# Optimization experiments

Measured on AMD Instinct MI355X. Metric: run time of the kernel, lower is better.

## Reference

```python
import jax, jax.numpy as jnp
import numpy as np
from jax import lax

KH, KW = 3, 3
STRIDE = 1
PAD = 1


def setup_inputs() -> dict:
    key = jax.random.key(0)
    k1, k2, k3 = jax.random.split(key, 3)
    x = jax.random.normal(k1, (16, 256, 56, 56), dtype=jnp.float32)
    # pruned weight after reinit_weight(): shape (n_kept, out_c)
    weight = jax.random.normal(k2, (1152, 256), dtype=jnp.float32) * 0.05
    # kept im2col row indices (sorted, in [0, C*kh*kw))
    idx = jnp.sort(jax.random.randint(k3, (1152,), 0, 256 * KH * KW)).astype(jnp.int32)
    return {"x": x, "weight": weight, "idx": idx}


def reference(x, weight, idx):
    N, C, H, W = x.shape
    out_h = (H + 2 * PAD - KH) // STRIDE + 1
    out_w = (W + 2 * PAD - KW) // STRIDE + 1
    out_c = weight.shape[1]
    # im2col: patches is [N, C*KH*KW, out_h, out_w]; channel flatten order is
    # (C, kh, kw), matching the original permute(1, 4, 5, 0, 2, 3).
    patches = lax.conv_general_dilated_patches(
        x, (KH, KW), (STRIDE, STRIDE), [(PAD, PAD), (PAD, PAD)]
    )
    col = patches.transpose(1, 0, 2, 3).reshape(C * KH * KW, N * out_h * out_w)
    # prune rows (irregular gather) then GEMM with pruned weight
    x_tile = col[idx, :].T                      # [N*out_h*out_w, n_kept]
    conv_out = x_tile @ weight                  # [N*out_h*out_w, out_c]
    # reshape to NCHW as in original
    out = conv_out.reshape(N, out_h * out_w, out_c).transpose(0, 2, 1)
    return out.reshape(N, out_c, out_h, out_w)
```

## Files before the change

kernel.cpp:

```cpp
#include <hip/hip_runtime.h>

typedef __attribute__((ext_vector_type(8))) short short8;
typedef __attribute__((ext_vector_type(4))) float f32x4;
typedef __attribute__((ext_vector_type(4))) int i32x4;

typedef __attribute__((address_space(1))) const unsigned int gas_u32;
typedef __attribute__((address_space(3))) unsigned int las_u32;

#define HW 56
#define P_IMG 3136
#define XSTRIDE 802816
#define OUT_C 256
#define K_TOT 1152
#define KT_N 18
#define BM 128
#define NBLK 392

__device__ __forceinline__ unsigned short f2bf_bits(float f) {
    unsigned u = __builtin_bit_cast(unsigned, f);
    return (unsigned short)((u + 0x7FFFu + ((u >> 16) & 1u)) >> 16);
}

__global__ __launch_bounds__(256) void prep_w_kernel(const float* __restrict__ w,
                                                     unsigned short* __restrict__ gw) {
    int i = blockIdx.x * 256 + threadIdx.x;
    int e = i & 63;
    int oc = (i >> 6) & 255;
    int t = i >> 14;
    int ksrc = t * 64 + (e ^ ((oc & 7) << 3));
    gw[i] = f2bf_bits(w[ksrc * 256 + oc]);
}

__global__ __launch_bounds__(256) void prep_idx_kernel(const int* __restrict__ idx,
                                                       int* __restrict__ didx) {
    int i = blockIdx.x * 256 + threadIdx.x;
    if (i < K_TOT) {
        int v = idx[i];
        int c = v / 9;
        int rr = v - c * 9;
        int dh = rr / 3;
        int dw = rr - dh * 3;
        int delta_b = c * P_IMG + (dh - 1) * HW + (dw - 1) + 57;
        didx[i] = delta_b | (rr << 20);
    }
}

__global__ __launch_bounds__(512, 2) void mconv_mfma(
        const float* __restrict__ x,
        const unsigned short* __restrict__ gw,
        const int* __restrict__ didx,
        float* __restrict__ out) {
    __shared__ __attribute__((aligned(16))) char smem[98304];
    char* const A0 = smem;
    char* const A1 = smem + 16384;
    char* const W0 = smem + 32768;
    char* const W1 = smem + 65536;

    const int tid = threadIdx.x;
    const int wv  = tid >> 6;
    const int ln  = tid & 63;
    const int lhi = ln >> 4;
    const int llo = ln & 15;
    const int oc0 = (wv >> 1) * 64;
    const int mw0 = (wv & 1) * 64;

    const int bid = blockIdx.x;
    const int m0 = ((bid & 7) * 49 + (bid >> 3)) * BM;

    const int sr = tid >> 2;
    const int sq = tid & 3;
    const int mrow = m0 + sr;
    const int nimg = mrow / P_IMG;
    const int p = mrow - nimg * P_IMG;
    const int oh = p / HW;
    const int ow = p - oh * HW;
    const int gbase = nimg * XSTRIDE + p - 57;
    const int ohm1 = oh - 1, owm1 = ow - 1;

    unsigned oklut = 0;
    #pragma unroll
    for (int dh = 0; dh < 3; ++dh)
        #pragma unroll
        for (int dw = 0; dw < 3; ++dw) {
            bool okh = (unsigned)(ohm1 + dh) < (unsigned)HW;
            bool okw = (unsigned)(owm1 + dw) < (unsigned)HW;
            if (okh && okw) oklut |= (1u << (dh * 3 + dw));
        }

    {
        float tv[16];
        unsigned okm = 0;
        const int kbase = sq * 16;
        #pragma unroll
        for (int q4 = 0; q4 < 4; ++q4) {
            i32x4 d = *(const i32x4*)(didx + kbase + q4 * 4);
            int vvv[4] = { d.x, d.y, d.z, d.w };
            #pragma unroll
            for (int jj = 0; jj < 4; ++jj) {
                int j = q4 * 4 + jj;
                int v = vvv[jj];
                int addr = gbase + (v & 0xFFFFF);
                unsigned ok = (oklut >> (v >> 20)) & 1u;
                tv[j] = x[ok ? addr : 0];
                okm |= ok << j;
            }
        }
        #pragma unroll
        for (int rd = 0; rd < 4; ++rd) {
            const char* g = (const char*)gw + rd * 8192 + tid * 16;
            __builtin_amdgcn_global_load_lds((gas_u32*)g, (las_u32*)(W0 + rd * 8192 + tid * 16), 16, 0, 0);
        }
        short8 pk0, pk1;
        #pragma unroll
        for (int j = 0; j < 8; ++j) {
            pk0[j] = (short)(((okm >> j) & 1u) ? f2bf_bits(tv[j]) : (unsigned short)0);
            pk1[j] = (short)(((okm >> (j + 8)) & 1u) ? f2bf_bits(tv[j + 8]) : (unsigned short)0);
        }
        const int swz = (sr & 7) << 4;
        char* rowp = A0 + sr * 128;
        *(short8*)(rowp + ((sq * 32) ^ swz)) = pk0;
        *(short8*)(rowp + ((sq * 32 + 16) ^ swz)) = pk1;
    }
    __syncthreads();

    f32x4 acc[4][4] = {};

    for (int kt = 0; kt < KT_N; ++kt) {
        char* const Ac = (kt & 1) ? A1 : A0;
        char* const An = (kt & 1) ? A0 : A1;
        char* const Wc = (kt & 1) ? W1 : W0;
        char* const Wn = (kt & 1) ? W0 : W1;

        float tv[16];
        unsigned okm = 0;
        const bool do_stage = (kt + 1 < KT_N);
        if (do_stage) {
            const int kbase = (kt + 1) * 64 + sq * 16;
            #pragma unroll
            for (int q4 = 0; q4 < 4; ++q4) {
                i32x4 d = *(const i32x4*)(didx + kbase + q4 * 4);
                int vvv[4] = { d.x, d.y, d.z, d.w };
                #pragma unroll
                for (int jj = 0; jj < 4; ++jj) {
                    int j = q4 * 4 + jj;
                    int v = vvv[jj];
                    int addr = gbase + (v & 0xFFFFF);
                    unsigned ok = (oklut >> (v >> 20)) & 1u;
                    tv[j] = x[ok ? addr : 0];
                    okm |= ok << j;
                }
            }
            #pragma unroll
            for (int rd = 0; rd < 4; ++rd) {
                const char* g = (const char*)gw + (kt + 1) * 32768 + rd * 8192 + tid * 16;
                __builtin_amdgcn_global_load_lds((gas_u32*)g, (las_u32*)(Wn + rd * 8192 + tid * 16), 16, 0, 0);
            }
        }
        __builtin_amdgcn_sched_barrier(0);

        #pragma unroll
        for (int ks = 0; ks < 2; ++ks) {
            short8 wf[4], af[4];
            #pragma unroll
            for (int i = 0; i < 4; ++i) {
                const int row = oc0 + i * 16 + llo;
                wf[i] = *(const short8*)(Wc + row * 128 + ((ks * 64 + lhi * 16) ^ ((row & 7) << 4)));
            }
            #pragma unroll
            for (int i = 0; i < 4; ++i) {
                const int row = mw0 + i * 16 + llo;
                af[i] = *(const short8*)(Ac + row * 128 + ((ks * 64 + lhi * 16) ^ ((row & 7) << 4)));
            }
            #pragma unroll
            for (int ni = 0; ni < 4; ++ni)
                #pragma unroll
                for (int mi = 0; mi < 4; ++mi)
                    acc[ni][mi] = __builtin_amdgcn_mfma_f32_16x16x32_bf16(wf[ni], af[mi], acc[ni][mi], 0, 0, 0);
        }

        if (do_stage) {
            short8 pk0, pk1;
            #pragma unroll
            for (int j = 0; j < 8; ++j) {
                pk0[j] = (short)(((okm >> j) & 1u) ? f2bf_bits(tv[j]) : (unsigned short)0);
                pk1[j] = (short)(((okm >> (j + 8)) & 1u) ? f2bf_bits(tv[j + 8]) : (unsigned short)0);
            }
            const int swz = (sr & 7) << 4;
            char* rowp = An + sr * 128;
            *(short8*)(rowp + ((sq * 32) ^ swz)) = pk0;
            *(short8*)(rowp + ((sq * 32 + 16) ^ swz)) = pk1;
        }
        __syncthreads();
    }

    #pragma unroll
    for (int mi = 0; mi < 4; ++mi) {
        const int mg = m0 + mw0 + mi * 16 + llo;
        const int n = mg / P_IMG;
        const int pp = mg - n * P_IMG;
        float* ob = out + n * XSTRIDE + pp;
        #pragma unroll
        for (int ni = 0; ni < 4; ++ni) {
            const int ocb = (oc0 + ni * 16 + lhi * 4) * P_IMG;
            #pragma unroll
            for (int j = 0; j < 4; ++j)
                ob[ocb + j * P_IMG] = acc[ni][mi][j];
        }
    }
}

extern "C" void kernel_launch(void* const* d_in, const int* in_sizes, int n_in,
                              void* d_out, int out_size, void* d_ws, size_t ws_size,
                              hipStream_t stream) {
    const float* x  = (const float*)d_in[0];
    const float* w  = (const float*)d_in[1];
    const int* idx  = (const int*)d_in[2];
    float* out = (float*)d_out;

    unsigned short* gw = (unsigned short*)d_ws;
    int* didx = (int*)((char*)d_ws + K_TOT * OUT_C * 2);

    prep_w_kernel<<<dim3(1152), dim3(256), 0, stream>>>(w, gw);
    prep_idx_kernel<<<dim3(5), dim3(256), 0, stream>>>(idx, didx);
    mconv_mfma<<<dim3(NBLK), dim3(512), 0, stream>>>(x, gw, didx, out);
}
```

Baseline: 189.5 us.

## Halve M tile, read weight fragments straight from global, drop weight LDS staging

The M tile per block shrinks from 128 to 64 rows and the grid doubles to 784 blocks. Shared memory drops from 96KB to 16KB and the launch bound now asks for 4 blocks per CU. Weight fragments are no longer staged into LDS with global_load_lds; the prep kernel writes them in an MFMA-fragment-friendly packed layout and each wave loads them directly from global/L2 every k-step. The aim is higher occupancy and less LDS traffic and footprint, at the cost of more repeated global weight reads and lower MFMA reuse per A-tile.

```diff
diff --git a/kernel.cpp b/kernel.cpp
--- a/kernel.cpp
+++ b/kernel.cpp
@@ -3,9 +3,6 @@
 typedef __attribute__((ext_vector_type(8))) short short8;
 typedef __attribute__((ext_vector_type(4))) float f32x4;
 typedef __attribute__((ext_vector_type(4))) int i32x4;
-
-typedef __attribute__((address_space(1))) const unsigned int gas_u32;
-typedef __attribute__((address_space(3))) unsigned int las_u32;
 
 #define HW 56
 #define P_IMG 3136
@@ -13,8 +10,8 @@
 #define OUT_C 256
 #define K_TOT 1152
 #define KT_N 18
-#define BM 128
-#define NBLK 392
+#define BM 64
+#define NBLK 784
 
 __device__ __forceinline__ unsigned short f2bf_bits(float f) {
     unsigned u = __builtin_bit_cast(unsigned, f);
@@ -24,11 +21,13 @@
 __global__ __launch_bounds__(256) void prep_w_kernel(const float* __restrict__ w,
                                                      unsigned short* __restrict__ gw) {
     int i = blockIdx.x * 256 + threadIdx.x;
-    int e = i & 63;
-    int oc = (i >> 6) & 255;
-    int t = i >> 14;
-    int ksrc = t * 64 + (e ^ ((oc & 7) << 3));
-    gw[i] = f2bf_bits(w[ksrc * 256 + oc]);
+    int oc = i & 255;
+    int s = i >> 8;
+    short8 pk;
+    #pragma unroll
+    for (int j = 0; j < 8; ++j)
+        pk[j] = (short)f2bf_bits(w[(s * 8 + j) * 256 + oc]);
+    *(short8*)(gw + s * 2048 + oc * 8) = pk;
 }
 
 __global__ __launch_bounds__(256) void prep_idx_kernel(const int* __restrict__ idx,
@@ -45,16 +44,14 @@
     }
 }
 
-__global__ __launch_bounds__(512, 2) void mconv_mfma(
+__global__ __launch_bounds__(512, 4) void mconv_mfma(
         const float* __restrict__ x,
         const unsigned short* __restrict__ gw,
         const int* __restrict__ didx,
         float* __restrict__ out) {
-    __shared__ __attribute__((aligned(16))) char smem[98304];
+    __shared__ __attribute__((aligned(16))) char smem[16384];
     char* const A0 = smem;
-    char* const A1 = smem + 16384;
-    char* const W0 = smem + 32768;
-    char* const W1 = smem + 65536;
+    char* const A1 = smem + 8192;
 
     const int tid = threadIdx.x;
     const int wv  = tid >> 6;
@@ -62,13 +59,13 @@
     const int lhi = ln >> 4;
     const int llo = ln & 15;
     const int oc0 = (wv >> 1) * 64;
-    const int mw0 = (wv & 1) * 64;
+    const int mw0 = (wv & 1) * 32;
 
     const int bid = blockIdx.x;
-    const int m0 = ((bid & 7) * 49 + (bid >> 3)) * BM;
+    const int m0 = ((bid & 7) * 98 + (bid >> 3)) * BM;
 
-    const int sr = tid >> 2;
-    const int sq = tid & 3;
+    const int sr = tid >> 3;
+    const int sq = tid & 7;
     const int mrow = m0 + sr;
     const int nimg = mrow / P_IMG;
     const int p = mrow - nimg * P_IMG;
@@ -87,114 +84,90 @@
             if (okh && okw) oklut |= (1u << (dh * 3 + dw));
         }
 
+    const int swz = (sr & 7) << 4;
+    char* const rowp0 = A0 + sr * 128;
+    char* const rowp1 = A1 + sr * 128;
+
     {
-        float tv[16];
+        float tv[8];
         unsigned okm = 0;
-        const int kbase = sq * 16;
+        const int kbase = sq * 8;
+        i32x4 d0 = *(const i32x4*)(didx + kbase);
+        i32x4 d1 = *(const i32x4*)(didx + kbase + 4);
+        int vv[8] = { d0.x, d0.y, d0.z, d0.w, d1.x, d1.y, d1.z, d1.w };
         #pragma unroll
-        for (int q4 = 0; q4 < 4; ++q4) {
-            i32x4 d = *(const i32x4*)(didx + kbase + q4 * 4);
-            int vvv[4] = { d.x, d.y, d.z, d.w };
+        for (int j = 0; j < 8; ++j) {
+            int v = vv[j];
+            int addr = gbase + (v & 0xFFFFF);
+            unsigned ok = (oklut >> (v >> 20)) & 1u;
+            tv[j] = x[ok ? addr : 0];
+            okm |= ok << j;
+        }
+        short8 pk;
+        #pragma unroll
+        for (int j = 0; j < 8; ++j)
+            pk[j] = (short)(((okm >> j) & 1u) ? f2bf_bits(tv[j]) : (unsigned short)0);
+        *(short8*)(rowp0 + ((sq * 16) ^ swz)) = pk;
+    }
+    __syncthreads();
+
+    f32x4 acc[4][2] = {};
+
+    for (int kt = 0; kt < KT_N; ++kt) {
+        char* const Ac = (kt & 1) ? A1 : A0;
+        char* const rowpn = (kt & 1) ? rowp0 : rowp1;
+
+        float tv[8];
+        unsigned okm = 0;
+        const bool do_stage = (kt + 1 < KT_N);
+        if (do_stage) {
+            const int kbase = (kt + 1) * 64 + sq * 8;
+            i32x4 d0 = *(const i32x4*)(didx + kbase);
+            i32x4 d1 = *(const i32x4*)(didx + kbase + 4);
+            int vv[8] = { d0.x, d0.y, d0.z, d0.w, d1.x, d1.y, d1.z, d1.w };
             #pragma unroll
-            for (int jj = 0; jj < 4; ++jj) {
-                int j = q4 * 4 + jj;
-                int v = vvv[jj];
+            for (int j = 0; j < 8; ++j) {
+                int v = vv[j];
                 int addr = gbase + (v & 0xFFFFF);
                 unsigned ok = (oklut >> (v >> 20)) & 1u;
                 tv[j] = x[ok ? addr : 0];
                 okm |= ok << j;
             }
         }
-        #pragma unroll
-        for (int rd = 0; rd < 4; ++rd) {
-            const char* g = (const char*)gw + rd * 8192 + tid * 16;
-            __builtin_amdgcn_global_load_lds((gas_u32*)g, (las_u32*)(W0 + rd * 8192 + tid * 16), 16, 0, 0);
-        }
-        short8 pk0, pk1;
-        #pragma unroll
-        for (int j = 0; j < 8; ++j) {
-            pk0[j] = (short)(((okm >> j) & 1u) ? f2bf_bits(tv[j]) : (unsigned short)0);
-            pk1[j] = (short)(((okm >> (j + 8)) & 1u) ? f2bf_bits(tv[j + 8]) : (unsigned short)0);
-        }
-        const int swz = (sr & 7) << 4;
-        char* rowp = A0 + sr * 128;
-        *(short8*)(rowp + ((sq * 32) ^ swz)) = pk0;
-        *(short8*)(rowp + ((sq * 32 + 16) ^ swz)) = pk1;
-    }
-    __syncthreads();
-
-    f32x4 acc[4][4] = {};
-
-    for (int kt = 0; kt < KT_N; ++kt) {
-        char* const Ac = (kt & 1) ? A1 : A0;
-        char* const An = (kt & 1) ? A0 : A1;
-        char* const Wc = (kt & 1) ? W1 : W0;
-        char* const Wn = (kt & 1) ? W0 : W1;
-
-        float tv[16];
-        unsigned okm = 0;
-        const bool do_stage = (kt + 1 < KT_N);
-        if (do_stage) {
-            const int kbase = (kt + 1) * 64 + sq * 16;
-            #pragma unroll
-            for (int q4 = 0; q4 < 4; ++q4) {
-                i32x4 d = *(const i32x4*)(didx + kbase + q4 * 4);
-                int vvv[4] = { d.x, d.y, d.z, d.w };
-                #pragma unroll
-                for (int jj = 0; jj < 4; ++jj) {
-                    int j = q4 * 4 + jj;
-                    int v = vvv[jj];
-                    int addr = gbase + (v & 0xFFFFF);
-                    unsigned ok = (oklut >> (v >> 20)) & 1u;
-                    tv[j] = x[ok ? addr : 0];
-                    okm |= ok << j;
-                }
-            }
-            #pragma unroll
-            for (int rd = 0; rd < 4; ++rd) {
-                const char* g = (const char*)gw + (kt + 1) * 32768 + rd * 8192 + tid * 16;
-                __builtin_amdgcn_global_load_lds((gas_u32*)g, (las_u32*)(Wn + rd * 8192 + tid * 16), 16, 0, 0);
-            }
-        }
         __builtin_amdgcn_sched_barrier(0);
 
         #pragma unroll
         for (int ks = 0; ks < 2; ++ks) {
-            short8 wf[4], af[4];
+            short8 wf[4], af[2];
             #pragma unroll
             for (int i = 0; i < 4; ++i) {
                 const int row = oc0 + i * 16 + llo;
-                wf[i] = *(const short8*)(Wc + row * 128 + ((ks * 64 + lhi * 16) ^ ((row & 7) << 4)));
+                wf[i] = *(const short8*)(gw + (kt * 8 + ks * 4 + lhi) * 2048 + row * 8);
             }
             #pragma unroll
-            for (int i = 0; i < 4; ++i) {
+            for (int i = 0; i < 2; ++i) {
                 const int row = mw0 + i * 16 + llo;
                 af[i] = *(const short8*)(Ac + row * 128 + ((ks * 64 + lhi * 16) ^ ((row & 7) << 4)));
             }
             #pragma unroll
             for (int ni = 0; ni < 4; ++ni)
                 #pragma unroll
-                for (int mi = 0; mi < 4; ++mi)
+                for (int mi = 0; mi < 2; ++mi)
                     acc[ni][mi] = __builtin_amdgcn_mfma_f32_16x16x32_bf16(wf[ni], af[mi], acc[ni][mi], 0, 0, 0);
         }
 
         if (do_stage) {
-            short8 pk0, pk1;
+            short8 pk;
             #pragma unroll
-            for (int j = 0; j < 8; ++j) {
-                pk0[j] = (short)(((okm >> j) & 1u) ? f2bf_bits(tv[j]) : (unsigned short)0);
-                pk1[j] = (short)(((okm >> (j + 8)) & 1u) ? f2bf_bits(tv[j + 8]) : (unsigned short)0);
-            }
-            const int swz = (sr & 7) << 4;
-            char* rowp = An + sr * 128;
-            *(short8*)(rowp + ((sq * 32) ^ swz)) = pk0;
-            *(short8*)(rowp + ((sq * 32 + 16) ^ swz)) = pk1;
+            for (int j = 0; j < 8; ++j)
+                pk[j] = (short)(((okm >> j) & 1u) ? f2bf_bits(tv[j]) : (unsigned short)0);
+            *(short8*)(rowpn + ((sq * 16) ^ swz)) = pk;
         }
         __syncthreads();
     }
 
     #pragma unroll
-    for (int mi = 0; mi < 4; ++mi) {
+    for (int mi = 0; mi < 2; ++mi) {
         const int mg = m0 + mw0 + mi * 16 + llo;
         const int n = mg / P_IMG;
         const int pp = mg - n * P_IMG;
@@ -220,7 +193,7 @@
     unsigned short* gw = (unsigned short*)d_ws;
     int* didx = (int*)((char*)d_ws + K_TOT * OUT_C * 2);
 
-    prep_w_kernel<<<dim3(1152), dim3(256), 0, stream>>>(w, gw);
+    prep_w_kernel<<<dim3(144), dim3(256), 0, stream>>>(w, gw);
     prep_idx_kernel<<<dim3(5), dim3(256), 0, stream>>>(idx, didx);
     mconv_mfma<<<dim3(NBLK), dim3(512), 0, stream>>>(x, gw, didx, out);
 }
```

New measurement: 222.5 us. +17.4%, slower.
